# Kernel tuning notes

Measured on AMD Instinct MI355X. Metric: run time of the kernel, lower is better.

The kernel has to match this reference:

```python
import jax, jax.numpy as jnp
import numpy as np

EPS = 1e-5

def lrelu(x):
    return jnp.where(x >= 0, x, 0.1 * x)

def bn_eval(x, g, b, m, v):
    # eval-mode BatchNorm over the last (channel) axis
    return (x - m) * (g * jax.lax.rsqrt(v + EPS)) + b

def setup_inputs():
    key = jax.random.key(0)
    ks = jax.random.split(key, 12)
    Nq, K, Cin, Fc, Co = 20000, 32, 3, 64, 64
    q_points = jax.random.normal(ks[0], (Nq, Cin), jnp.float32)
    s_points = jax.random.normal(ks[1], (Nq, Cin), jnp.float32)
    feat = jax.random.normal(ks[2], (Nq, Fc), jnp.float32)
    # valid indices 0..Nq (Nq == shadow/pad row appended in forward)
    neighb_inds = jax.random.randint(ks[3], (Nq, K), 0, Nq + 1)
    def w(k, shape, fan_in):
        return jax.random.normal(k, shape, jnp.float32) / np.float32(np.sqrt(fan_in))
    W_pos2 = w(ks[4], (Fc, Cin), Cin)          # convpos2: Conv2d(Cin, Fc, 1)
    W_attn = w(ks[5], (Co * Cin, Fc), Fc)      # convattn: Conv2d(Fc, Co*Cin, 1)
    W_res = w(ks[6], (Co, Fc), Fc)             # residual 1x1 conv
    def bn(k, c):
        k1, k2, k3, k4 = jax.random.split(k, 4)
        return (jax.random.normal(k1, (c,), jnp.float32) * 0.1 + 1.0,
                jax.random.normal(k2, (c,), jnp.float32) * 0.1,
                jax.random.normal(k3, (c,), jnp.float32) * 0.1,
                jax.random.uniform(k4, (c,), jnp.float32) * 0.5 + 0.5)
    bq = bn(ks[7], Fc); bp = bn(ks[8], Cin); b1 = bn(ks[9], Co); br = bn(ks[10], Co)
    return dict(q_points=q_points, s_points=s_points, neighb_inds=neighb_inds, feat=feat,
                W_pos2=W_pos2, W_attn=W_attn, W_res=W_res,
                bnq_g=bq[0], bnq_b=bq[1], bnq_m=bq[2], bnq_v=bq[3],
                bnp_g=bp[0], bnp_b=bp[1], bnp_m=bp[2], bnp_v=bp[3],
                bn1_g=b1[0], bn1_b=b1[1], bn1_m=b1[2], bn1_v=b1[3],
                bnr_g=br[0], bnr_b=br[1], bnr_m=br[2], bnr_v=br[3])

def reference(q_points, s_points, neighb_inds, feat, W_pos2, W_attn, W_res,
              bnq_g, bnq_b, bnq_m, bnq_v, bnp_g, bnp_b, bnp_m, bnp_v,
              bn1_g, bn1_b, bn1_m, bn1_v, bnr_g, bnr_b, bnr_m, bnr_v):
    Nq, Cin = q_points.shape
    Fc = feat.shape[1]
    Co = W_res.shape[0]
    K = neighb_inds.shape[1]
    # append shadow (zero) row for out-of-range neighbor indices
    s_pad = jnp.concatenate([s_points, jnp.zeros((1, Cin), s_points.dtype)], 0)
    f_pad = jnp.concatenate([feat, jnp.zeros((1, Fc), feat.dtype)], 0)
    xg = s_pad[neighb_inds]                      # [Nq,K,Cin] EFR_P gather
    yg = f_pad[neighb_inds]                      # [Nq,K,Fc]  EFR_F gather
    x_v = xg - q_points[:, None, :]              # [Nq,K,Cin] values
    x_q = lrelu(bn_eval(feat, bnq_g, bnq_b, bnq_m, bnq_v))          # [Nq,Fc]
    pos0 = lrelu(bn_eval(s_points, bnp_g, bnp_b, bnp_m, bnp_v))     # [Nq,Cin]
    pos = (pos0[:, None, :] - x_v) @ W_pos2.T                       # [Nq,K,Fc]
    attn = x_q[:, None, :] - yg + pos                               # [Nq,K,Fc]
    attn = jax.nn.softmax(attn / jnp.sqrt(jnp.float32(Fc)), axis=1) # softmax over K
    attn = (attn @ W_attn.T).reshape(Nq, K, Co, Cin)                # [Nq,K,Co,Cin]
    y_e = jnp.einsum('nkoi,nki->nko', attn, x_v)                    # [Nq,K,Co]
    y_e = lrelu(bn_eval(y_e, bn1_g, bn1_b, bn1_m, bn1_v))
    res = bn_eval(yg @ W_res.T, bnr_g, bnr_b, bnr_m, bnr_v)         # [Nq,K,Co]
    y_e = lrelu(y_e + res)
    return y_e.max(axis=1)                                          # [Nq,Co]
```

## Files before the change

kernel.cpp:

```cpp
#include <hip/hip_runtime.h>
#include <math.h>

#define KNB 32
#define FC 64
#define CO 64
#define EPS 1e-5f
#define NBLOCKS 1024

typedef __attribute__((ext_vector_type(8))) short short8;
typedef __attribute__((ext_vector_type(4))) float floatx4;

__device__ __forceinline__ unsigned int pkbf(float a, float b) {
    unsigned int ua = (__float_as_uint(a) + 0x8000u) >> 16;
    unsigned int ub = (__float_as_uint(b) + 0x8000u) & 0xFFFF0000u;
    return ua | ub;
}
__device__ __forceinline__ short f2bf(float x) {
    return (short)((__float_as_uint(x) + 0x8000u) >> 16);
}
__device__ __forceinline__ float lrelu(float x) { return fmaxf(x, 0.1f * x); }

__global__ __launch_bounds__(256, 4) void GCT_61272003445298_kernel(
    const float* __restrict__ q_points,
    const float* __restrict__ s_points,
    const int*   __restrict__ neighb,
    const float* __restrict__ feat,
    const float* __restrict__ W_pos2,
    const float* __restrict__ W_attn,
    const float* __restrict__ W_res,
    const float* __restrict__ bnq_g, const float* __restrict__ bnq_b,
    const float* __restrict__ bnq_m, const float* __restrict__ bnq_v,
    const float* __restrict__ bnp_g, const float* __restrict__ bnp_b,
    const float* __restrict__ bnp_m, const float* __restrict__ bnp_v,
    const float* __restrict__ bn1_g, const float* __restrict__ bn1_b,
    const float* __restrict__ bn1_m, const float* __restrict__ bn1_v,
    const float* __restrict__ bnr_g, const float* __restrict__ bnr_b,
    const float* __restrict__ bnr_m, const float* __restrict__ bnr_v,
    float* __restrict__ out, int Nq)
{
    const int t = threadIdx.x;
    const int wv = t >> 6;
    const int lane = t & 63;
    const int cc = lane & 15, quad = lane >> 4;
    const int o = wv * 16 + cc;

    __shared__ __align__(16) short sA1[64 * 72];
    __shared__ __align__(16) short sA2[64 * 72];
    __shared__ float sXv[64][4];
    __shared__ __align__(16) float sXqc[2][64];
    __shared__ __align__(16) float sWp2[192];
    __shared__ float sQs[64], sQb[64];
    __shared__ float sPs[4], sPb[4];
    __shared__ int   sIdx[64];

    if (t < 192) sWp2[t] = 0.125f * W_pos2[t];
    if (t < 64) {
        float sc = bnq_g[t] * rsqrtf(bnq_v[t] + EPS);
        sQs[t] = sc; sQb[t] = bnq_b[t] - bnq_m[t] * sc;
        if (t < 3) {
            float scp = bnp_g[t] * rsqrtf(bnp_v[t] + EPS);
            sPs[t] = scp; sPb[t] = bnp_b[t] - bnp_m[t] * scp;
        }
    }
    const float e1s = bn1_g[o] * rsqrtf(bn1_v[o] + EPS);
    const float e1b = bn1_b[o] - bn1_m[o] * e1s;
    const float ers = bnr_g[o] * rsqrtf(bnr_v[o] + EPS);
    const float erb = bnr_b[o] - bnr_m[o] * ers;

    short8 bW[4][2];
    #pragma unroll
    for (int ty = 0; ty < 4; ++ty) {
        const float* wrow = (ty < 3) ? (W_attn + (long)(o * 3 + ty) * FC)
                                     : (W_res  + (long)o * FC);
        #pragma unroll
        for (int ks = 0; ks < 2; ++ks) {
            int k0 = ks * 32 + quad * 8;
            float4 w0 = *(const float4*)(wrow + k0);
            float4 w1 = *(const float4*)(wrow + k0 + 4);
            short8 b;
            b[0] = f2bf(w0.x); b[1] = f2bf(w0.y); b[2] = f2bf(w0.z); b[3] = f2bf(w0.w);
            b[4] = f2bf(w1.x); b[5] = f2bf(w1.y); b[6] = f2bf(w1.z); b[7] = f2bf(w1.w);
            bW[ty][ks] = b;
        }
    }
    __syncthreads();

    const int fq = t & 15, rbase = t >> 4;
    float wp[12];
    *(float4*)&wp[0] = *(const float4*)&sWp2[fq * 12];
    *(float4*)&wp[4] = *(const float4*)&sWp2[fq * 12 + 4];
    *(float4*)&wp[8] = *(const float4*)&sWp2[fq * 12 + 8];

    const int npair = (Nq + 1) >> 1;
    for (int p = blockIdx.x; p < npair; p += NBLOCKS) {
        const long n0 = 2L * p;
        long n1 = n0 + 1;
        const bool has1 = (n1 < Nq);
        if (!has1) n1 = n0;

        if (t < 64) {
            int q = t >> 5;
            long nn = q ? n1 : n0;
            int idx = neighb[nn * KNB + (t & 31)];
            sIdx[t] = idx;
            float q0 = q_points[nn * 3 + 0];
            float q1v = q_points[nn * 3 + 1];
            float q2 = q_points[nn * 3 + 2];
            float x0 = 0.f, x1 = 0.f, x2 = 0.f;
            if (idx < Nq) {
                x0 = s_points[(long)idx * 3 + 0];
                x1 = s_points[(long)idx * 3 + 1];
                x2 = s_points[(long)idx * 3 + 2];
            }
            sXv[t][0] = x0 - q0; sXv[t][1] = x1 - q1v; sXv[t][2] = x2 - q2;
        } else if (t >= 192) {
            int f = t - 192;
            float xq0 = lrelu(fmaf(feat[n0 * FC + f], sQs[f], sQb[f]));
            float xq1 = lrelu(fmaf(feat[n1 * FC + f], sQs[f], sQb[f]));
            float c0 = 0.125f * xq0, c1 = 0.125f * xq1;
            #pragma unroll
            for (int i = 0; i < 3; ++i) {
                float p0 = lrelu(fmaf(s_points[n0 * 3 + i], sPs[i], sPb[i]));
                float p1 = lrelu(fmaf(s_points[n1 * 3 + i], sPs[i], sPb[i]));
                float w = sWp2[f * 3 + i];
                c0 = fmaf(p0, w, c0);
                c1 = fmaf(p1, w, c1);
            }
            sXqc[0][f] = c0; sXqc[1][f] = c1;
        }
        __syncthreads();

        {
            float4 xqc0 = *(const float4*)&sXqc[0][fq * 4];
            float4 xqc1 = *(const float4*)&sXqc[1][fq * 4];
            #pragma unroll
            for (int it = 0; it < 4; ++it) {
                int row = it * 16 + rbase;
                float4 xqc = (it < 2) ? xqc0 : xqc1;
                int idx = sIdx[row];
                float4 y = make_float4(0.f, 0.f, 0.f, 0.f);
                if (idx < Nq) y = *(const float4*)(feat + (long)idx * FC + fq * 4);
                uint2 pk; pk.x = pkbf(y.x, y.y); pk.y = pkbf(y.z, y.w);
                *(uint2*)(sA2 + row * 72 + fq * 4) = pk;
                float4 xv = *(const float4*)&sXv[row][0];
                float l0 = fmaf(y.x, -0.125f, xqc.x);
                l0 = fmaf(-xv.x, wp[0], l0); l0 = fmaf(-xv.y, wp[1], l0); l0 = fmaf(-xv.z, wp[2], l0);
                float l1 = fmaf(y.y, -0.125f, xqc.y);
                l1 = fmaf(-xv.x, wp[3], l1); l1 = fmaf(-xv.y, wp[4], l1); l1 = fmaf(-xv.z, wp[5], l1);
                float l2 = fmaf(y.z, -0.125f, xqc.z);
                l2 = fmaf(-xv.x, wp[6], l2); l2 = fmaf(-xv.y, wp[7], l2); l2 = fmaf(-xv.z, wp[8], l2);
                float l3 = fmaf(y.w, -0.125f, xqc.w);
                l3 = fmaf(-xv.x, wp[9], l3); l3 = fmaf(-xv.y, wp[10], l3); l3 = fmaf(-xv.z, wp[11], l3);
                uint2 pl; pl.x = pkbf(l0, l1); pl.y = pkbf(l2, l3);
                *(uint2*)(sA1 + row * 72 + fq * 4) = pl;
            }
        }
        __syncthreads();

        {
            const int q = wv >> 1;
            const int f2 = ((wv & 1) << 4) + cc;
            short* base = sA1 + (q * 32 + quad * 2) * 72 + f2 * 2;
            const int roff[8] = {0, 1, 8, 9, 16, 17, 24, 25};
            float elo[8], ehi[8];
            float slo = 0.f, shi = 0.f;
            #pragma unroll
            for (int j = 0; j < 8; ++j) {
                unsigned u = *(const unsigned*)(base + roff[j] * 72);
                float flo = __uint_as_float(u << 16);
                float fhi = __uint_as_float(u & 0xFFFF0000u);
                elo[j] = __expf(flo); ehi[j] = __expf(fhi);
                slo += elo[j]; shi += ehi[j];
            }
            slo += __shfl_xor(slo, 16); slo += __shfl_xor(slo, 32);
            shi += __shfl_xor(shi, 16); shi += __shfl_xor(shi, 32);
            float ilo = 1.f / slo, ihi = 1.f / shi;
            #pragma unroll
            for (int j = 0; j < 8; ++j)
                *(unsigned*)(base + roff[j] * 72) = pkbf(elo[j] * ilo, ehi[j] * ihi);
        }
        __syncthreads();

        float m0 = -1e30f, m1 = -1e30f;
        #pragma unroll
        for (int mt = 0; mt < 4; ++mt) {
            floatx4 acc[4];
            #pragma unroll
            for (int ty = 0; ty < 4; ++ty) acc[ty] = (floatx4){0.f, 0.f, 0.f, 0.f};
            int r0 = mt * 16 + cc;
            #pragma unroll
            for (int ks = 0; ks < 2; ++ks) {
                int kof = ks * 32 + quad * 8;
                short8 a1 = *(const short8*)(sA1 + r0 * 72 + kof);
                short8 a2 = *(const short8*)(sA2 + r0 * 72 + kof);
                acc[0] = __builtin_amdgcn_mfma_f32_16x16x32_bf16(a1, bW[0][ks], acc[0], 0, 0, 0);
                acc[1] = __builtin_amdgcn_mfma_f32_16x16x32_bf16(a1, bW[1][ks], acc[1], 0, 0, 0);
                acc[2] = __builtin_amdgcn_mfma_f32_16x16x32_bf16(a1, bW[2][ks], acc[2], 0, 0, 0);
                acc[3] = __builtin_amdgcn_mfma_f32_16x16x32_bf16(a2, bW[3][ks], acc[3], 0, 0, 0);
            }
            #pragma unroll
            for (int reg = 0; reg < 4; ++reg) {
                int r = mt * 16 + quad * 4 + reg;
                float4 xv = *(const float4*)&sXv[r][0];
                float y = acc[0][reg] * xv.x + acc[1][reg] * xv.y + acc[2][reg] * xv.z;
                float ybn = lrelu(y * e1s + e1b);
                float rbn = acc[3][reg] * ers + erb;
                float v = lrelu(ybn + rbn);
                if (mt < 2) m0 = fmaxf(m0, v); else m1 = fmaxf(m1, v);
            }
        }
        m0 = fmaxf(m0, __shfl_xor(m0, 16));
        m0 = fmaxf(m0, __shfl_xor(m0, 32));
        m1 = fmaxf(m1, __shfl_xor(m1, 16));
        m1 = fmaxf(m1, __shfl_xor(m1, 32));
        if (lane < 16) {
            out[n0 * CO + o] = m0;
            if (has1) out[n1 * CO + o] = m1;
        }
        __syncthreads();
    }
}

extern "C" void kernel_launch(void* const* d_in, const int* in_sizes, int n_in,
                              void* d_out, int out_size, void* d_ws, size_t ws_size,
                              hipStream_t stream) {
    const float* q_points = (const float*)d_in[0];
    const float* s_points = (const float*)d_in[1];
    const int*   neighb   = (const int*)  d_in[2];
    const float* feat     = (const float*)d_in[3];
    const float* W_pos2   = (const float*)d_in[4];
    const float* W_attn   = (const float*)d_in[5];
    const float* W_res    = (const float*)d_in[6];
    const float* bnq_g = (const float*)d_in[7];
    const float* bnq_b = (const float*)d_in[8];
    const float* bnq_m = (const float*)d_in[9];
    const float* bnq_v = (const float*)d_in[10];
    const float* bnp_g = (const float*)d_in[11];
    const float* bnp_b = (const float*)d_in[12];
    const float* bnp_m = (const float*)d_in[13];
    const float* bnp_v = (const float*)d_in[14];
    const float* bn1_g = (const float*)d_in[15];
    const float* bn1_b = (const float*)d_in[16];
    const float* bn1_m = (const float*)d_in[17];
    const float* bn1_v = (const float*)d_in[18];
    const float* bnr_g = (const float*)d_in[19];
    const float* bnr_b = (const float*)d_in[20];
    const float* bnr_m = (const float*)d_in[21];
    const float* bnr_v = (const float*)d_in[22];
    float* out = (float*)d_out;

    int Nq = in_sizes[0] / 3;

    hipLaunchKernelGGL(GCT_61272003445298_kernel,
                       dim3(NBLOCKS), dim3(256), 0, stream,
                       q_points, s_points, neighb, feat, W_pos2, W_attn, W_res,
                       bnq_g, bnq_b, bnq_m, bnq_v,
                       bnp_g, bnp_b, bnp_m, bnp_v,
                       bn1_g, bn1_b, bn1_m, bn1_v,
                       bnr_g, bnr_b, bnr_m, bnr_v,
                       out, Nq);
}
```

Before: 164.1 us.

## Fuse gather, logit, and softmax phases per thread to drop barriers

Reassigns threads so each one handles four neighbor rows for one query and four feature columns. Each thread now gathers its own indices, query features and point positions, and computes logits and the softmax exponentials in registers. Shuffle reductions over neighbors replace the separate shared-memory softmax pass, which removes two __syncthreads and the bf16 round-trip of the logits. It also folds log2(e)/8 into the constants so it can use exp2 and rcp intrinsics. The cost is redundant loads of q_points and s_points across threads, plus some added register pressure.

Measured after the change: 161.4 us. About the same (-1.7%).

```diff
diff --git a/kernel.cpp b/kernel.cpp
--- a/kernel.cpp
+++ b/kernel.cpp
@@ -6,9 +6,21 @@
 #define CO 64
 #define EPS 1e-5f
 #define NBLOCKS 1024
+#define CL 0.180336880095853f
 
 typedef __attribute__((ext_vector_type(8))) short short8;
 typedef __attribute__((ext_vector_type(4))) float floatx4;
+
+#if __has_builtin(__builtin_amdgcn_exp2f)
+#define EXP2F(x) __builtin_amdgcn_exp2f(x)
+#else
+#define EXP2F(x) exp2f(x)
+#endif
+#if __has_builtin(__builtin_amdgcn_rcpf)
+#define RCPF(x) __builtin_amdgcn_rcpf(x)
+#else
+#define RCPF(x) (1.f / (x))
+#endif
 
 __device__ __forceinline__ unsigned int pkbf(float a, float b) {
     unsigned int ua = (__float_as_uint(a) + 0x8000u) >> 16;
@@ -44,23 +56,26 @@
     const int cc = lane & 15, quad = lane >> 4;
     const int o = wv * 16 + cc;
 
+    const int qB  = t >> 7;
+    const int kg  = lane >> 3;
+    const int fqB = (((t >> 6) & 1) << 3) + (lane & 7);
+
     __shared__ __align__(16) short sA1[64 * 72];
     __shared__ __align__(16) short sA2[64 * 72];
     __shared__ float sXv[64][4];
-    __shared__ __align__(16) float sXqc[2][64];
     __shared__ __align__(16) float sWp2[192];
-    __shared__ float sQs[64], sQb[64];
-    __shared__ float sPs[4], sPb[4];
-    __shared__ int   sIdx[64];
-
-    if (t < 192) sWp2[t] = 0.125f * W_pos2[t];
+    __shared__ __align__(16) float sQs[64], sQb[64];
+
+    if (t < 192) sWp2[t] = CL * W_pos2[t];
     if (t < 64) {
         float sc = bnq_g[t] * rsqrtf(bnq_v[t] + EPS);
         sQs[t] = sc; sQb[t] = bnq_b[t] - bnq_m[t] * sc;
-        if (t < 3) {
-            float scp = bnp_g[t] * rsqrtf(bnp_v[t] + EPS);
-            sPs[t] = scp; sPb[t] = bnp_b[t] - bnp_m[t] * scp;
-        }
+    }
+    float ps[3], pb[3];
+    #pragma unroll
+    for (int i = 0; i < 3; ++i) {
+        float sc = bnp_g[i] * rsqrtf(bnp_v[i] + EPS);
+        ps[i] = sc; pb[i] = bnp_b[i] - bnp_m[i] * sc;
     }
     const float e1s = bn1_g[o] * rsqrtf(bn1_v[o] + EPS);
     const float e1b = bn1_b[o] - bn1_m[o] * e1s;
@@ -85,11 +100,13 @@
     }
     __syncthreads();
 
-    const int fq = t & 15, rbase = t >> 4;
     float wp[12];
-    *(float4*)&wp[0] = *(const float4*)&sWp2[fq * 12];
-    *(float4*)&wp[4] = *(const float4*)&sWp2[fq * 12 + 4];
-    *(float4*)&wp[8] = *(const float4*)&sWp2[fq * 12 + 8];
+    *(float4*)&wp[0] = *(const float4*)&sWp2[fqB * 12];
+    *(float4*)&wp[4] = *(const float4*)&sWp2[fqB * 12 + 4];
+    *(float4*)&wp[8] = *(const float4*)&sWp2[fqB * 12 + 8];
+
+    const float4* __restrict__ feat4 = (const float4*)feat;
+    const bool xvWriter = ((t & 0x47) == 0);
 
     const int npair = (Nq + 1) >> 1;
     for (int p = blockIdx.x; p < npair; p += NBLOCKS) {
@@ -97,87 +114,74 @@
         long n1 = n0 + 1;
         const bool has1 = (n1 < Nq);
         if (!has1) n1 = n0;
-
-        if (t < 64) {
-            int q = t >> 5;
-            long nn = q ? n1 : n0;
-            int idx = neighb[nn * KNB + (t & 31)];
-            sIdx[t] = idx;
-            float q0 = q_points[nn * 3 + 0];
-            float q1v = q_points[nn * 3 + 1];
-            float q2 = q_points[nn * 3 + 2];
-            float x0 = 0.f, x1 = 0.f, x2 = 0.f;
-            if (idx < Nq) {
-                x0 = s_points[(long)idx * 3 + 0];
-                x1 = s_points[(long)idx * 3 + 1];
-                x2 = s_points[(long)idx * 3 + 2];
+        const long nn = qB ? n1 : n0;
+
+        float nqp0 = -q_points[nn * 3 + 0];
+        float nqp1 = -q_points[nn * 3 + 1];
+        float nqp2 = -q_points[nn * 3 + 2];
+        float p0 = lrelu(fmaf(s_points[nn * 3 + 0], ps[0], pb[0]));
+        float p1 = lrelu(fmaf(s_points[nn * 3 + 1], ps[1], pb[1]));
+        float p2 = lrelu(fmaf(s_points[nn * 3 + 2], ps[2], pb[2]));
+        int4 idx4 = *(const int4*)(neighb + nn * KNB + kg * 4);
+
+        float4 qs4 = *(const float4*)&sQs[fqB * 4];
+        float4 qb4 = *(const float4*)&sQb[fqB * 4];
+        float4 fx  = feat4[(int)(nn * 16) + fqB];
+        float4 xqc;
+        {
+            float x0 = lrelu(fmaf(fx.x, qs4.x, qb4.x));
+            float x1 = lrelu(fmaf(fx.y, qs4.y, qb4.y));
+            float x2 = lrelu(fmaf(fx.z, qs4.z, qb4.z));
+            float x3 = lrelu(fmaf(fx.w, qs4.w, qb4.w));
+            xqc.x = fmaf(p0, wp[0], fmaf(p1, wp[1],  fmaf(p2, wp[2],  CL * x0)));
+            xqc.y = fmaf(p0, wp[3], fmaf(p1, wp[4],  fmaf(p2, wp[5],  CL * x1)));
+            xqc.z = fmaf(p0, wp[6], fmaf(p1, wp[7],  fmaf(p2, wp[8],  CL * x2)));
+            xqc.w = fmaf(p0, wp[9], fmaf(p1, wp[10], fmaf(p2, wp[11], CL * x3)));
+        }
+
+        float ev[4][4];
+        float s0 = 0.f, s1 = 0.f, s2 = 0.f, s3 = 0.f;
+        #pragma unroll
+        for (int j = 0; j < 4; ++j) {
+            const int idx = ((const int*)&idx4)[j];
+            const int row = qB * 32 + kg * 4 + j;
+            const float sel = (idx < Nq) ? 1.f : 0.f;
+            const int idc = (idx < Nq) ? idx : 0;
+            float4 y = feat4[idc * 16 + fqB];
+            y.x *= sel; y.y *= sel; y.z *= sel; y.w *= sel;
+            uint2 pk; pk.x = pkbf(y.x, y.y); pk.y = pkbf(y.z, y.w);
+            *(uint2*)(sA2 + row * 72 + fqB * 4) = pk;
+            float xv0 = fmaf(s_points[idc * 3 + 0], sel, nqp0);
+            float xv1 = fmaf(s_points[idc * 3 + 1], sel, nqp1);
+            float xv2 = fmaf(s_points[idc * 3 + 2], sel, nqp2);
+            if (xvWriter) {
+                sXv[row][0] = xv0; sXv[row][1] = xv1; sXv[row][2] = xv2;
+                sXv[row][3] = 0.f;
             }
-            sXv[t][0] = x0 - q0; sXv[t][1] = x1 - q1v; sXv[t][2] = x2 - q2;
-        } else if (t >= 192) {
-            int f = t - 192;
-            float xq0 = lrelu(fmaf(feat[n0 * FC + f], sQs[f], sQb[f]));
-            float xq1 = lrelu(fmaf(feat[n1 * FC + f], sQs[f], sQb[f]));
-            float c0 = 0.125f * xq0, c1 = 0.125f * xq1;
-            #pragma unroll
-            for (int i = 0; i < 3; ++i) {
-                float p0 = lrelu(fmaf(s_points[n0 * 3 + i], sPs[i], sPb[i]));
-                float p1 = lrelu(fmaf(s_points[n1 * 3 + i], sPs[i], sPb[i]));
-                float w = sWp2[f * 3 + i];
-                c0 = fmaf(p0, w, c0);
-                c1 = fmaf(p1, w, c1);
-            }
-            sXqc[0][f] = c0; sXqc[1][f] = c1;
-        }
-        __syncthreads();
-
-        {
-            float4 xqc0 = *(const float4*)&sXqc[0][fq * 4];
-            float4 xqc1 = *(const float4*)&sXqc[1][fq * 4];
-            #pragma unroll
-            for (int it = 0; it < 4; ++it) {
-                int row = it * 16 + rbase;
-                float4 xqc = (it < 2) ? xqc0 : xqc1;
-                int idx = sIdx[row];
-                float4 y = make_float4(0.f, 0.f, 0.f, 0.f);
-                if (idx < Nq) y = *(const float4*)(feat + (long)idx * FC + fq * 4);
-                uint2 pk; pk.x = pkbf(y.x, y.y); pk.y = pkbf(y.z, y.w);
-                *(uint2*)(sA2 + row * 72 + fq * 4) = pk;
-                float4 xv = *(const float4*)&sXv[row][0];
-                float l0 = fmaf(y.x, -0.125f, xqc.x);
-                l0 = fmaf(-xv.x, wp[0], l0); l0 = fmaf(-xv.y, wp[1], l0); l0 = fmaf(-xv.z, wp[2], l0);
-                float l1 = fmaf(y.y, -0.125f, xqc.y);
-                l1 = fmaf(-xv.x, wp[3], l1); l1 = fmaf(-xv.y, wp[4], l1); l1 = fmaf(-xv.z, wp[5], l1);
-                float l2 = fmaf(y.z, -0.125f, xqc.z);
-                l2 = fmaf(-xv.x, wp[6], l2); l2 = fmaf(-xv.y, wp[7], l2); l2 = fmaf(-xv.z, wp[8], l2);
-                float l3 = fmaf(y.w, -0.125f, xqc.w);
-                l3 = fmaf(-xv.x, wp[9], l3); l3 = fmaf(-xv.y, wp[10], l3); l3 = fmaf(-xv.z, wp[11], l3);
-                uint2 pl; pl.x = pkbf(l0, l1); pl.y = pkbf(l2, l3);
-                *(uint2*)(sA1 + row * 72 + fq * 4) = pl;
-            }
-        }
-        __syncthreads();
-
-        {
-            const int q = wv >> 1;
-            const int f2 = ((wv & 1) << 4) + cc;
-            short* base = sA1 + (q * 32 + quad * 2) * 72 + f2 * 2;
-            const int roff[8] = {0, 1, 8, 9, 16, 17, 24, 25};
-            float elo[8], ehi[8];
-            float slo = 0.f, shi = 0.f;
-            #pragma unroll
-            for (int j = 0; j < 8; ++j) {
-                unsigned u = *(const unsigned*)(base + roff[j] * 72);
-                float flo = __uint_as_float(u << 16);
-                float fhi = __uint_as_float(u & 0xFFFF0000u);
-                elo[j] = __expf(flo); ehi[j] = __expf(fhi);
-                slo += elo[j]; shi += ehi[j];
-            }
-            slo += __shfl_xor(slo, 16); slo += __shfl_xor(slo, 32);
-            shi += __shfl_xor(shi, 16); shi += __shfl_xor(shi, 32);
-            float ilo = 1.f / slo, ihi = 1.f / shi;
-            #pragma unroll
-            for (int j = 0; j < 8; ++j)
-                *(unsigned*)(base + roff[j] * 72) = pkbf(elo[j] * ilo, ehi[j] * ihi);
+            float l0 = fmaf(y.x, -CL, xqc.x);
+            l0 = fmaf(-xv0, wp[0], l0); l0 = fmaf(-xv1, wp[1], l0); l0 = fmaf(-xv2, wp[2], l0);
+            float l1 = fmaf(y.y, -CL, xqc.y);
+            l1 = fmaf(-xv0, wp[3], l1); l1 = fmaf(-xv1, wp[4], l1); l1 = fmaf(-xv2, wp[5], l1);
+            float l2 = fmaf(y.z, -CL, xqc.z);
+            l2 = fmaf(-xv0, wp[6], l2); l2 = fmaf(-xv1, wp[7], l2); l2 = fmaf(-xv2, wp[8], l2);
+            float l3 = fmaf(y.w, -CL, xqc.w);
+            l3 = fmaf(-xv0, wp[9], l3); l3 = fmaf(-xv1, wp[10], l3); l3 = fmaf(-xv2, wp[11], l3);
+            ev[j][0] = EXP2F(l0); ev[j][1] = EXP2F(l1);
+            ev[j][2] = EXP2F(l2); ev[j][3] = EXP2F(l3);
+            s0 += ev[j][0]; s1 += ev[j][1]; s2 += ev[j][2]; s3 += ev[j][3];
+        }
+        s0 += __shfl_xor(s0, 8); s0 += __shfl_xor(s0, 16); s0 += __shfl_xor(s0, 32);
+        s1 += __shfl_xor(s1, 8); s1 += __shfl_xor(s1, 16); s1 += __shfl_xor(s1, 32);
+        s2 += __shfl_xor(s2, 8); s2 += __shfl_xor(s2, 16); s2 += __shfl_xor(s2, 32);
+        s3 += __shfl_xor(s3, 8); s3 += __shfl_xor(s3, 16); s3 += __shfl_xor(s3, 32);
+        const float i0 = RCPF(s0), i1 = RCPF(s1), i2 = RCPF(s2), i3 = RCPF(s3);
+        #pragma unroll
+        for (int j = 0; j < 4; ++j) {
+            const int row = qB * 32 + kg * 4 + j;
+            uint2 pw;
+            pw.x = pkbf(ev[j][0] * i0, ev[j][1] * i1);
+            pw.y = pkbf(ev[j][2] * i2, ev[j][3] * i3);
+            *(uint2*)(sA1 + row * 72 + fqB * 4) = pw;
         }
         __syncthreads();
 
```
